# Optimization experiments

Measured on AMD Instinct MI355X. Metric: run time of the kernel, lower is better.

## Reference

```python
import jax, jax.numpy as jnp
import numpy as np
from jax import lax


def _gauss_kernel(size=5, sigma=1.0):
    ax = np.arange(size, dtype=np.float64) - size // 2
    g = np.exp(-(ax ** 2) / (2.0 * sigma ** 2))
    k = np.outer(g, g)
    k /= k.sum()
    return jnp.asarray(k, jnp.float32)[None, None]  # [1,1,5,5]


_GAUSS = _gauss_kernel()
_SOBEL_X = jnp.asarray([[-1, 0, 1], [-2, 0, 2], [-1, 0, 1]], jnp.float32)[None, None]
_SOBEL_Y = jnp.asarray([[-1, -2, -1], [0, 0, 0], [1, 2, 1]], jnp.float32)[None, None]

# 8 directional NMS filters: center minus neighbor, bin k <-> angle k*45 degrees.
# (row, col) neighbor offsets for angles 0,45,...,315.
_OFFS = [(0, 1), (-1, 1), (-1, 0), (-1, -1), (0, -1), (1, -1), (1, 0), (1, 1)]
_dir = np.zeros((8, 1, 3, 3), np.float32)
for _i, (_dr, _dc) in enumerate(_OFFS):
    _dir[_i, 0, 1, 1] = 1.0
    _dir[_i, 0, 1 + _dr, 1 + _dc] = -1.0
_DIR = jnp.asarray(_dir)


def _conv(x, k):
    # x: [B,1,H,W], k: [O,1,kh,kw] -> [B,O,H,W] (same padding, stride 1)
    return lax.conv_general_dilated(
        x, k, (1, 1), 'SAME', dimension_numbers=('NCHW', 'OIHW', 'NCHW'))


def canny(img):
    """Canny pipeline: blur -> sobel -> magnitude/orientation -> angle-binned NMS.
    img: [B,1,H,W]. Returns (thin_edges [B,1,H,W], orientation_deg [B,1,H,W])."""
    blurred = _conv(img, _GAUSS)
    gx = _conv(blurred, _SOBEL_X)
    gy = _conv(blurred, _SOBEL_Y)
    mag = jnp.sqrt(gx * gx + gy * gy + 1e-12)
    # orientation in [0,360], quantized to 45-degree bins
    ori = jnp.round((jnp.degrees(jnp.arctan2(gy, gx)) + 180.0) / 45.0) * 45.0
    idx_pos = (ori / 45.0).astype(jnp.int32) % 8          # [B,1,H,W]
    idx_neg = (idx_pos + 4) % 8
    diffs = _conv(mag, _DIR)                              # [B,8,H,W] center-minus-neighbor
    d_pos = jnp.take_along_axis(diffs, idx_pos, axis=1)   # along gradient direction
    d_neg = jnp.take_along_axis(diffs, idx_neg, axis=1)   # opposite direction
    is_max = (jnp.minimum(d_pos, d_neg) > 0.0).astype(mag.dtype)
    thin_edges = mag * is_max
    return thin_edges, ori


def reference(X, Y):
    grad_t, ori_t = canny(X)
    grad_p, ori_p = canny(Y)
    # per-sample L1 (mean) then summed over the batch, matching the python loop
    e1 = jnp.abs(grad_t - grad_p).mean(axis=(1, 2, 3)).sum()
    e2 = jnp.abs(ori_t - ori_p).mean(axis=(1, 2, 3)).sum()
    return e1 + e2


def setup_inputs() -> dict:
    key = jax.random.key(0)
    k1, k2 = jax.random.split(key)
    B, C, H, W = 16, 1, 512, 512
    X = jax.random.normal(k1, (B, C, H, W), dtype=jnp.float32)
    Y = jax.random.normal(k2, (B, C, H, W), dtype=jnp.float32)
    return {"X": X, "Y": Y}
```

## Files before the change

kernel.cpp:

```cpp
#include <hip/hip_runtime.h>
#include <cmath>

#define HH 512
#define WW 512
#define TW 64
#define TH 64
#define SW 68
#define HB_R 72
#define BL_R 68
#define MG_R 66
#define NT 256
#define NIT 5

#define NG_A (HB_R * 17)
#define NG_B (BL_R * 17)
#define NG_C (MG_R * 17)

struct Blur5 { float w[5]; };

#define DR_PACK 43265u
#define DC_PACK 36890u

__device__ __forceinline__ float4 ld4(const float* p) {
  return *reinterpret_cast<const float4*>(p);
}
__device__ __forceinline__ void st4(float* p, float4 v) {
  *reinterpret_cast<float4*>(p) = v;
}

__device__ __forceinline__ int orient_bin(float gx, float gy) {
  const float T1 = 0.41421356237309503f;
  const float T2 = 2.41421356237309503f;
  float a = fabsf(gy), b = fabsf(gx);
  int sx = (int)(__float_as_uint(gx) >> 31);
  int sy = (int)(__float_as_uint(gy) >> 31);
  int rc;
  if (a <= T1 * b)      rc = sx ? (8 - 8 * sy) : 4;
  else if (a >= T2 * b) rc = 6 - 4 * sy;
  else                  rc = sx ? (7 - 6 * sy) : (5 - 2 * sy);
  return rc;
}

template<bool INTERIOR>
__device__ __forceinline__ float canny_tile_loss(
    const float* __restrict__ xb, const float* __restrict__ yb,
    int base_r, int base_c, float* __restrict__ rX, float* __restrict__ rY,
    const Blur5& kb)
{
  const int tid = threadIdx.x;
  const float k0 = kb.w[0], k1 = kb.w[1], k2 = kb.w[2], k3 = kb.w[3], k4 = kb.w[4];

  #pragma unroll
  for (int it = 0; it < NIT; ++it) {
    int g = tid + it * NT;
    if (g < NG_A) {
      int hr = (int)((unsigned)g / 17u), k = g - hr * 17;
      int gr = base_r + hr - 4;
      int gcb = base_c + k * 4 - 4;
      const float* px = xb + gr * WW + gcb;
      const float* py = yb + gr * WW + gcb;
      float4 xa = {0,0,0,0}, xc = {0,0,0,0}, ya = {0,0,0,0}, yc = {0,0,0,0};
      if (INTERIOR) {
        xa = ld4(px); ya = ld4(py);
        xc = ld4(px + 4); yc = ld4(py + 4);
      } else {
        bool rok = (unsigned)gr < HH;
        bool ok0 = rok && (unsigned)gcb < WW;
        bool ok1 = rok && (unsigned)(gcb + 4) < WW;
        if (ok0) { xa = ld4(px); ya = ld4(py); }
        if (ok1) { xc = ld4(px + 4); yc = ld4(py + 4); }
      }
      float4 ox, oy;
      ox.x = k0*xa.x + k1*xa.y + k2*xa.z + k3*xa.w + k4*xc.x;
      ox.y = k0*xa.y + k1*xa.z + k2*xa.w + k3*xc.x + k4*xc.y;
      ox.z = k0*xa.z + k1*xa.w + k2*xc.x + k3*xc.y + k4*xc.z;
      ox.w = k0*xa.w + k1*xc.x + k2*xc.y + k3*xc.z + k4*xc.w;
      oy.x = k0*ya.x + k1*ya.y + k2*ya.z + k3*ya.w + k4*yc.x;
      oy.y = k0*ya.y + k1*ya.z + k2*ya.w + k3*yc.x + k4*yc.y;
      oy.z = k0*ya.z + k1*ya.w + k2*yc.x + k3*yc.y + k4*yc.z;
      oy.w = k0*ya.w + k1*yc.x + k2*yc.y + k3*yc.z + k4*yc.w;
      st4(&rX[hr * SW + k * 4], ox);
      st4(&rY[hr * SW + k * 4], oy);
    }
  }
  __syncthreads();

  float4 bx[NIT], by[NIT];
  #pragma unroll
  for (int it = 0; it < NIT; ++it) {
    int g = tid + it * NT;
    if (g < NG_B) {
      int br = (int)((unsigned)g / 17u), k = g - br * 17, c4 = k * 4;
      bool c0 = true, c1 = true, c2 = true, c3 = true;
      if (!INTERIOR) {
        bool rok = (unsigned)(base_r + br - 2) < HH;
        int gcb = base_c + c4 - 2;
        c0 = rok && (unsigned)(gcb + 0) < WW;
        c1 = rok && (unsigned)(gcb + 1) < WW;
        c2 = rok && (unsigned)(gcb + 2) < WW;
        c3 = rok && (unsigned)(gcb + 3) < WW;
      }
      {
        const float* p = &rX[br * SW + c4];
        float4 v0 = ld4(p), v1 = ld4(p + SW), v2 = ld4(p + 2*SW),
               v3 = ld4(p + 3*SW), v4 = ld4(p + 4*SW);
        float4 o;
        o.x = c0 ? (k0*v0.x + k1*v1.x + k2*v2.x + k3*v3.x + k4*v4.x) : 0.f;
        o.y = c1 ? (k0*v0.y + k1*v1.y + k2*v2.y + k3*v3.y + k4*v4.y) : 0.f;
        o.z = c2 ? (k0*v0.z + k1*v1.z + k2*v2.z + k3*v3.z + k4*v4.z) : 0.f;
        o.w = c3 ? (k0*v0.w + k1*v1.w + k2*v2.w + k3*v3.w + k4*v4.w) : 0.f;
        bx[it] = o;
      }
      {
        const float* p = &rY[br * SW + c4];
        float4 v0 = ld4(p), v1 = ld4(p + SW), v2 = ld4(p + 2*SW),
               v3 = ld4(p + 3*SW), v4 = ld4(p + 4*SW);
        float4 o;
        o.x = c0 ? (k0*v0.x + k1*v1.x + k2*v2.x + k3*v3.x + k4*v4.x) : 0.f;
        o.y = c1 ? (k0*v0.y + k1*v1.y + k2*v2.y + k3*v3.y + k4*v4.y) : 0.f;
        o.z = c2 ? (k0*v0.z + k1*v1.z + k2*v2.z + k3*v3.z + k4*v4.z) : 0.f;
        o.w = c3 ? (k0*v0.w + k1*v1.w + k2*v2.w + k3*v3.w + k4*v4.w) : 0.f;
        by[it] = o;
      }
    }
  }
  __syncthreads();
  #pragma unroll
  for (int it = 0; it < NIT; ++it) {
    int g = tid + it * NT;
    if (g < NG_B) {
      int br = (int)((unsigned)g / 17u), k = g - br * 17, c4 = k * 4;
      st4(&rX[br * SW + c4], bx[it]);
      st4(&rY[br * SW + c4], by[it]);
    }
  }
  __syncthreads();

  float4 mx[NIT], my[NIT];
  unsigned rcpx[NIT], rcpy[NIT];
  #pragma unroll
  for (int it = 0; it < NIT; ++it) {
    int g = tid + it * NT;
    if (g < NG_C) {
      int mr = (int)((unsigned)g / 17u), k = g - mr * 17, c4 = k * 4;
      bool rok = true;
      int gcb = base_c + c4 - 1;
      if (!INTERIOR) rok = (unsigned)(base_r + mr - 1) < HH;
      {
        const float* p = &rX[mr * SW + c4];
        float4 a0 = ld4(p),          b0 = ld4(p + 4);
        float4 a1 = ld4(p + SW),     b1 = ld4(p + SW + 4);
        float4 a2 = ld4(p + 2*SW),   b2 = ld4(p + 2*SW + 4);
        float e0[6] = {a0.x,a0.y,a0.z,a0.w,b0.x,b0.y};
        float e1[6] = {a1.x,a1.y,a1.z,a1.w,b1.x,b1.y};
        float e2[6] = {a2.x,a2.y,a2.z,a2.w,b2.x,b2.y};
        float4 o; float* po = &o.x;
        unsigned pk = 0;
        #pragma unroll
        for (int j = 0; j < 4; ++j) {
          float gx = (e0[j+2]-e0[j]) + 2.f*(e1[j+2]-e1[j]) + (e2[j+2]-e2[j]);
          float gy = (e2[j]-e0[j]) + 2.f*(e2[j+1]-e0[j+1]) + (e2[j+2]-e0[j+2]);
          pk |= (unsigned)orient_bin(gx, gy) << (8 * j);
          float m = sqrtf(gx*gx + gy*gy + 1e-12f);
          if (INTERIOR) po[j] = m;
          else po[j] = (rok && (unsigned)(gcb + j) < WW) ? m : 0.f;
        }
        mx[it] = o; rcpx[it] = pk;
      }
      {
        const float* p = &rY[mr * SW + c4];
        float4 a0 = ld4(p),          b0 = ld4(p + 4);
        float4 a1 = ld4(p + SW),     b1 = ld4(p + SW + 4);
        float4 a2 = ld4(p + 2*SW),   b2 = ld4(p + 2*SW + 4);
        float e0[6] = {a0.x,a0.y,a0.z,a0.w,b0.x,b0.y};
        float e1[6] = {a1.x,a1.y,a1.z,a1.w,b1.x,b1.y};
        float e2[6] = {a2.x,a2.y,a2.z,a2.w,b2.x,b2.y};
        float4 o; float* po = &o.x;
        unsigned pk = 0;
        #pragma unroll
        for (int j = 0; j < 4; ++j) {
          float gx = (e0[j+2]-e0[j]) + 2.f*(e1[j+2]-e1[j]) + (e2[j+2]-e2[j]);
          float gy = (e2[j]-e0[j]) + 2.f*(e2[j+1]-e0[j+1]) + (e2[j+2]-e0[j+2]);
          pk |= (unsigned)orient_bin(gx, gy) << (8 * j);
          float m = sqrtf(gx*gx + gy*gy + 1e-12f);
          if (INTERIOR) po[j] = m;
          else po[j] = (rok && (unsigned)(gcb + j) < WW) ? m : 0.f;
        }
        my[it] = o; rcpy[it] = pk;
      }
    }
  }
  __syncthreads();
  #pragma unroll
  for (int it = 0; it < NIT; ++it) {
    int g = tid + it * NT;
    if (g < NG_C) {
      int mr = (int)((unsigned)g / 17u), k = g - mr * 17, c4 = k * 4;
      st4(&rX[mr * SW + c4], mx[it]);
      st4(&rY[mr * SW + c4], my[it]);
    }
  }
  __syncthreads();

  float s = 0.f; int so = 0;
  #pragma unroll
  for (int it = 0; it < NIT; ++it) {
    int g = tid + it * NT;
    if (g < NG_C) {
      int mr = (int)((unsigned)g / 17u), k = g - mr * 17, c4 = k * 4;
      bool rowv = (unsigned)(mr - 1) < (unsigned)TH;
      const float* mcx = &mx[it].x;
      const float* mcy = &my[it].x;
      #pragma unroll
      for (int j = 0; j < 4; ++j) {
        int bj = c4 - 1 + j;
        bool valid = rowv && ((unsigned)bj < (unsigned)TW);
        int ci = mr * SW + c4 + j;
        int rcx = (int)((rcpx[it] >> (8 * j)) & 255u);
        int ip = rcx & 7;
        int dr = (int)((DR_PACK >> (2 * ip)) & 3u) - 1;
        int dc = (int)((DC_PACK >> (2 * ip)) & 3u) - 1;
        int off = dr * SW + dc;
        float mcv = mcx[j];
        float n1 = rX[ci + off];
        float n2 = rX[ci - off];
        float thx = (fminf(mcv - n1, mcv - n2) > 0.f) ? mcv : 0.f;
        int rcy = (int)((rcpy[it] >> (8 * j)) & 255u);
        ip = rcy & 7;
        dr = (int)((DR_PACK >> (2 * ip)) & 3u) - 1;
        dc = (int)((DC_PACK >> (2 * ip)) & 3u) - 1;
        off = dr * SW + dc;
        float mcw = mcy[j];
        float m1 = rY[ci + off];
        float m2 = rY[ci - off];
        float thy = (fminf(mcw - m1, mcw - m2) > 0.f) ? mcw : 0.f;
        s += valid ? fabsf(thx - thy) : 0.f;
        so += valid ? abs(rcx - rcy) : 0;
      }
    }
  }
  return s + 45.f * (float)so;
}

__global__ void __launch_bounds__(NT)
canny_loss_kernel(const float* __restrict__ X, const float* __restrict__ Y,
                  float* __restrict__ out, Blur5 kb)
{
  __shared__ float reg[2 * HB_R * SW];
  __shared__ float red[NT / 64];
  float* rX = reg;
  float* rY = reg + HB_R * SW;

  const int idx = blockIdx.x;
  const int b  = idx >> 6;
  const int tr = (idx >> 3) & 7;
  const int tc = idx & 7;
  const int base_r = tr * TH;
  const int base_c = tc * TW;
  const float* xb = X + (size_t)b * HH * WW;
  const float* yb = Y + (size_t)b * HH * WW;

  const bool interior = (tr >= 1) & (tr <= 6) & (tc >= 1) & (tc <= 6);
  float s = interior
      ? canny_tile_loss<true >(xb, yb, base_r, base_c, rX, rY, kb)
      : canny_tile_loss<false>(xb, yb, base_r, base_c, rX, rY, kb);

  #pragma unroll
  for (int off = 32; off >= 1; off >>= 1) s += __shfl_down(s, off, 64);
  const int tid = threadIdx.x;
  const int lane = tid & 63, wv = tid >> 6;
  if (lane == 0) red[wv] = s;
  __syncthreads();
  if (tid == 0) {
    float t = red[0] + red[1] + red[2] + red[3];
    atomicAdd(out, t * (1.0f / ((float)HH * (float)WW)));
  }
}

extern "C" void kernel_launch(void* const* d_in, const int* in_sizes, int n_in,
                              void* d_out, int out_size, void* d_ws, size_t ws_size,
                              hipStream_t stream)
{
  const float* X = (const float*)d_in[0];
  const float* Y = (const float*)d_in[1];
  float* out = (float*)d_out;

  hipMemsetAsync(out, 0, (size_t)out_size * sizeof(float), stream);

  Blur5 kb;
  {
    double g[5], ssum = 0.0;
    for (int i = 0; i < 5; ++i) { double d = i - 2; g[i] = std::exp(-(d * d) / 2.0); ssum += g[i]; }
    for (int i = 0; i < 5; ++i) kb.w[i] = (float)(g[i] / ssum);
  }

  canny_loss_kernel<<<1024, NT, 0, stream>>>(X, Y, out, kb);
}
```

Before: 40.30 us.

## Halve tile height, double threads, add separate blur buffer to drop syncs

Tile height drops from 64 to 32 rows and threads per block go from 256 to 512, which doubles the grid to 2048 blocks and cuts per-thread iterations from 5 to 2. A separate shared-memory buffer now holds the blur output, so the blur and magnitude stages write directly instead of staging results in registers behind an extra barrier. Two __syncthreads per tile are removed and register pressure is lower. In exchange, halo overhead rises (40 halo rows per 32 output rows instead of 72 per 64), so each block does proportionally more redundant loading and compute.

```diff
diff --git a/kernel.cpp b/kernel.cpp
--- a/kernel.cpp
+++ b/kernel.cpp
@@ -4,13 +4,13 @@
 #define HH 512
 #define WW 512
 #define TW 64
-#define TH 64
+#define TH 32
 #define SW 68
-#define HB_R 72
-#define BL_R 68
-#define MG_R 66
-#define NT 256
-#define NIT 5
+#define HB_R 40
+#define BL_R 36
+#define MG_R 34
+#define NT 512
+#define NIT 2
 
 #define NG_A (HB_R * 17)
 #define NG_B (BL_R * 17)
@@ -44,7 +44,9 @@
 template<bool INTERIOR>
 __device__ __forceinline__ float canny_tile_loss(
     const float* __restrict__ xb, const float* __restrict__ yb,
-    int base_r, int base_c, float* __restrict__ rX, float* __restrict__ rY,
+    int base_r, int base_c,
+    float* __restrict__ rX, float* __restrict__ rY,
+    float* __restrict__ blX, float* __restrict__ blY,
     const Blur5& kb)
 {
   const int tid = threadIdx.x;
@@ -85,7 +87,6 @@
   }
   __syncthreads();
 
-  float4 bx[NIT], by[NIT];
   #pragma unroll
   for (int it = 0; it < NIT; ++it) {
     int g = tid + it * NT;
@@ -109,7 +110,7 @@
         o.y = c1 ? (k0*v0.y + k1*v1.y + k2*v2.y + k3*v3.y + k4*v4.y) : 0.f;
         o.z = c2 ? (k0*v0.z + k1*v1.z + k2*v2.z + k3*v3.z + k4*v4.z) : 0.f;
         o.w = c3 ? (k0*v0.w + k1*v1.w + k2*v2.w + k3*v3.w + k4*v4.w) : 0.f;
-        bx[it] = o;
+        st4(&blX[br * SW + c4], o);
       }
       {
         const float* p = &rY[br * SW + c4];
@@ -120,18 +121,8 @@
         o.y = c1 ? (k0*v0.y + k1*v1.y + k2*v2.y + k3*v3.y + k4*v4.y) : 0.f;
         o.z = c2 ? (k0*v0.z + k1*v1.z + k2*v2.z + k3*v3.z + k4*v4.z) : 0.f;
         o.w = c3 ? (k0*v0.w + k1*v1.w + k2*v2.w + k3*v3.w + k4*v4.w) : 0.f;
-        by[it] = o;
-      }
-    }
-  }
-  __syncthreads();
-  #pragma unroll
-  for (int it = 0; it < NIT; ++it) {
-    int g = tid + it * NT;
-    if (g < NG_B) {
-      int br = (int)((unsigned)g / 17u), k = g - br * 17, c4 = k * 4;
-      st4(&rX[br * SW + c4], bx[it]);
-      st4(&rY[br * SW + c4], by[it]);
+        st4(&blY[br * SW + c4], o);
+      }
     }
   }
   __syncthreads();
@@ -147,7 +138,7 @@
       int gcb = base_c + c4 - 1;
       if (!INTERIOR) rok = (unsigned)(base_r + mr - 1) < HH;
       {
-        const float* p = &rX[mr * SW + c4];
+        const float* p = &blX[mr * SW + c4];
         float4 a0 = ld4(p),          b0 = ld4(p + 4);
         float4 a1 = ld4(p + SW),     b1 = ld4(p + SW + 4);
         float4 a2 = ld4(p + 2*SW),   b2 = ld4(p + 2*SW + 4);
@@ -166,9 +157,10 @@
           else po[j] = (rok && (unsigned)(gcb + j) < WW) ? m : 0.f;
         }
         mx[it] = o; rcpx[it] = pk;
-      }
-      {
-        const float* p = &rY[mr * SW + c4];
+        st4(&rX[mr * SW + c4], o);
+      }
+      {
+        const float* p = &blY[mr * SW + c4];
         float4 a0 = ld4(p),          b0 = ld4(p + 4);
         float4 a1 = ld4(p + SW),     b1 = ld4(p + SW + 4);
         float4 a2 = ld4(p + 2*SW),   b2 = ld4(p + 2*SW + 4);
@@ -187,17 +179,8 @@
           else po[j] = (rok && (unsigned)(gcb + j) < WW) ? m : 0.f;
         }
         my[it] = o; rcpy[it] = pk;
-      }
-    }
-  }
-  __syncthreads();
-  #pragma unroll
-  for (int it = 0; it < NIT; ++it) {
-    int g = tid + it * NT;
-    if (g < NG_C) {
-      int mr = (int)((unsigned)g / 17u), k = g - mr * 17, c4 = k * 4;
-      st4(&rX[mr * SW + c4], mx[it]);
-      st4(&rY[mr * SW + c4], my[it]);
+        st4(&rY[mr * SW + c4], o);
+      }
     }
   }
   __syncthreads();
@@ -246,24 +229,27 @@
 canny_loss_kernel(const float* __restrict__ X, const float* __restrict__ Y,
                   float* __restrict__ out, Blur5 kb)
 {
-  __shared__ float reg[2 * HB_R * SW];
+  __shared__ float hbmag[2 * HB_R * SW];
+  __shared__ float blbuf[2 * BL_R * SW];
   __shared__ float red[NT / 64];
-  float* rX = reg;
-  float* rY = reg + HB_R * SW;
+  float* rX  = hbmag;
+  float* rY  = hbmag + HB_R * SW;
+  float* blX = blbuf;
+  float* blY = blbuf + BL_R * SW;
 
   const int idx = blockIdx.x;
-  const int b  = idx >> 6;
-  const int tr = (idx >> 3) & 7;
+  const int b  = idx >> 7;
+  const int tr = (idx >> 3) & 15;
   const int tc = idx & 7;
   const int base_r = tr * TH;
   const int base_c = tc * TW;
   const float* xb = X + (size_t)b * HH * WW;
   const float* yb = Y + (size_t)b * HH * WW;
 
-  const bool interior = (tr >= 1) & (tr <= 6) & (tc >= 1) & (tc <= 6);
+  const bool interior = (tr >= 1) & (tr <= 14) & (tc >= 1) & (tc <= 6);
   float s = interior
-      ? canny_tile_loss<true >(xb, yb, base_r, base_c, rX, rY, kb)
-      : canny_tile_loss<false>(xb, yb, base_r, base_c, rX, rY, kb);
+      ? canny_tile_loss<true >(xb, yb, base_r, base_c, rX, rY, blX, blY, kb)
+      : canny_tile_loss<false>(xb, yb, base_r, base_c, rX, rY, blX, blY, kb);
 
   #pragma unroll
   for (int off = 32; off >= 1; off >>= 1) s += __shfl_down(s, off, 64);
@@ -272,7 +258,9 @@
   if (lane == 0) red[wv] = s;
   __syncthreads();
   if (tid == 0) {
-    float t = red[0] + red[1] + red[2] + red[3];
+    float t = 0.f;
+    #pragma unroll
+    for (int i = 0; i < NT / 64; ++i) t += red[i];
     atomicAdd(out, t * (1.0f / ((float)HH * (float)WW)));
   }
 }
@@ -294,5 +282,5 @@
     for (int i = 0; i < 5; ++i) kb.w[i] = (float)(g[i] / ssum);
   }
 
-  canny_loss_kernel<<<1024, NT, 0, stream>>>(X, Y, out, kb);
-}
+  canny_loss_kernel<<<2048, NT, 0, stream>>>(X, Y, out, kb);
+}
```

Measured after the change: 47.53 us. 1.18x slower.
